# Kernel tuning notes

Measured on AMD Instinct MI355X. Metric: run time of the kernel, lower is better.

Reference implementation:

```python
import jax, jax.numpy as jnp
import numpy as np
import math

B, N, DIM = 8, 8192, 256
DIM_ATTN, HEAD, RANK = 256, 4, 64
HEAD_DIM = DIM_ATTN // HEAD


def setup_inputs() -> dict:
    key = jax.random.key(0)
    ks = jax.random.split(key, 8)
    x = jax.random.normal(ks[0], (B, N, DIM), dtype=jnp.float32)
    z = jax.random.normal(ks[1], (B, N, DIM), dtype=jnp.float32)
    # nn.Linear(dim, dim_attn): weight (out,in) -> use (in,out) for x @ W
    Wq = jax.random.normal(ks[2], (DIM, DIM_ATTN), dtype=jnp.float32) / np.sqrt(DIM)
    bq = jnp.zeros((DIM_ATTN,), dtype=jnp.float32)
    K = jax.random.normal(ks[3], (RANK, HEAD, HEAD_DIM), dtype=jnp.float32)
    Wv = jax.random.normal(ks[4], (DIM, DIM), dtype=jnp.float32) / np.sqrt(DIM)
    bv = jnp.zeros((DIM,), dtype=jnp.float32)
    alpha = jnp.full((HEAD, 1), math.log(9.0), dtype=jnp.float32)
    beta = jnp.full((HEAD, 1), math.log(0.01), dtype=jnp.float32)
    return {"x": x, "z": z, "Wq": Wq, "bq": bq, "K": K, "Wv": Wv, "bv": bv,
            "alpha": alpha, "beta": beta}


def reference(x, z, Wq, bq, K, Wv, bv, alpha, beta):
    b, n, f = x.shape
    # q: (b, n, head, head_dim)
    q = (z @ Wq + bq).reshape(b, n, HEAD, HEAD_DIM)
    # attn scores over latent rank: (b, n, h, r)
    attn = jnp.einsum('bnhd,rhd->bnhr', q, K) / np.sqrt(HEAD_DIM).astype(np.float32)
    # value projection: (b, n, h, d)
    xv = (x @ Wv + bv).reshape(b, n, HEAD, HEAD_DIM)
    # pool over n with softmax over r: (b, r, h, d)
    pooled = jnp.einsum('bnhr,bnhd->brhd', jax.nn.softmax(attn, axis=-1), xv)
    # redistribute with softmax over n: (b, n, h, d)
    v = jnp.einsum('bnhr,brhd->bnhd', jax.nn.softmax(attn, axis=1), pooled)
    # sigmoid-gated combine; alpha/beta are (head, 1) broadcasting over (h, d)
    out = jax.nn.sigmoid(alpha) * xv + jax.nn.sigmoid(beta) * v
    return out.reshape(b, n, f)
```

## Files before the change

### kernel.cpp

```cpp
#include <hip/hip_runtime.h>
#include <hip/hip_bf16.h>

typedef __hip_bfloat16 bf16;
typedef __attribute__((ext_vector_type(8))) __bf16 bf16x8;
typedef __attribute__((ext_vector_type(4))) float f32x4;

#define BB 8
#define NN 8192
#define DIM 256
#define HEAD 4
#define HD 64
#define RANK 64
#define BN (BB*NN)

__device__ __forceinline__ float b2f(bf16 v){ return __bfloat162float(v); }
__device__ __forceinline__ bf16 f2b(float v){ return __float2bfloat16(v); }
__device__ __forceinline__ unsigned short f2bu(float f){
    bf16 h = __float2bfloat16(f);
    return *(unsigned short*)&h;
}
__device__ __forceinline__ float u2f(unsigned short u){
    unsigned int x = ((unsigned int)u) << 16; return __uint_as_float(x);
}
__device__ __forceinline__ __bf16 f2bb(float f){
    bf16 h = __float2bfloat16(f);
    return *reinterpret_cast<__bf16*>(&h);
}
__device__ __forceinline__ int swz(int k, int outer){
    return (((k >> 3) ^ (outer & 7)) << 3) | (k & 7);
}

__global__ void __launch_bounds__(256) kW(
    const float* __restrict__ Wq, const float* __restrict__ bq,
    const float* __restrict__ Km, const float* __restrict__ Wv,
    unsigned short* __restrict__ WattnT, unsigned short* __restrict__ WvT,
    float* __restrict__ battn)
{
    const int c = blockIdx.x;
    const int h = c >> 6, r = c & 63;
    const int t = threadIdx.x;
    __shared__ float Ks[64];
    if(t < 64) Ks[t] = Km[((size_t)r*HEAD + h)*64 + t];
    __syncthreads();

    const float* wqrow = Wq + (size_t)t*DIM + h*64;
    float a = 0.f;
    #pragma unroll
    for(int d = 0; d < 64; d++) a = fmaf(wqrow[d], Ks[d], a);
    WattnT[(size_t)c*DIM + t] = f2bu(0.125f * a);
    WvT[(size_t)c*DIM + t]    = f2bu(Wv[(size_t)t*DIM + c]);
    if(t == 0){
        float bb = 0.f;
        for(int d = 0; d < 64; d++) bb += bq[h*64+d]*Ks[d];
        battn[c] = 0.125f * bb;
    }
}

__global__ void __launch_bounds__(256) kA2(
    const float* __restrict__ A, const unsigned short* __restrict__ WT,
    const float* __restrict__ bias,
    float* __restrict__ outF, unsigned short* __restrict__ outB,
    float* __restrict__ Pm, float* __restrict__ Ps, const int bf16out)
{
    __shared__ __attribute__((aligned(16))) __bf16 As[64][40];
    __shared__ __attribute__((aligned(16))) __bf16 Ws[256][40];

    const int t    = threadIdx.x;
    const int lane = t & 63;
    const int w    = t >> 6;
    const int q    = lane >> 4;
    const int l15  = lane & 15;
    const int brow = blockIdx.x * 64;

    f32x4 acc[4][4];
    #pragma unroll
    for(int tm = 0; tm < 4; tm++)
        #pragma unroll
        for(int tn = 0; tn < 4; tn++) acc[tm][tn] = (f32x4){0.f,0.f,0.f,0.f};

    const int arow = t >> 2, aseg = t & 3;

    for(int k0 = 0; k0 < DIM; k0 += 32){
        {
            const float* ap = A + (size_t)(brow + arow)*DIM + k0 + aseg*8;
            float4 v0 = *(const float4*)(ap + 0);
            float4 v1 = *(const float4*)(ap + 4);
            __attribute__((aligned(16))) __bf16 tmp[8] = {
                f2bb(v0.x), f2bb(v0.y), f2bb(v0.z), f2bb(v0.w),
                f2bb(v1.x), f2bb(v1.y), f2bb(v1.z), f2bb(v1.w)};
            *(bf16x8*)&As[arow][aseg*8] = *(bf16x8*)tmp;
        }
        #pragma unroll
        for(int ii = 0; ii < 4; ii++){
            int c = t + 256*ii;
            int n = c >> 2, seg = c & 3;
            uint4 wv = *(const uint4*)(WT + (size_t)n*DIM + k0 + seg*8);
            *(uint4*)&Ws[n][seg*8] = wv;
        }
        __syncthreads();

        bf16x8 af[4], bf[4];
        #pragma unroll
        for(int tm = 0; tm < 4; tm++) af[tm] = *(const bf16x8*)&As[tm*16 + l15][q*8];
        #pragma unroll
        for(int tn = 0; tn < 4; tn++) bf[tn] = *(const bf16x8*)&Ws[w*64 + tn*16 + l15][q*8];
        #pragma unroll
        for(int tm = 0; tm < 4; tm++)
            #pragma unroll
            for(int tn = 0; tn < 4; tn++)
                acc[tm][tn] = __builtin_amdgcn_mfma_f32_16x16x32_bf16(
                    af[tm], bf[tn], acc[tm][tn], 0, 0, 0);
        __syncthreads();
    }

    if(bf16out){
        const int b  = brow >> 13;
        const int nb = brow & 8191;
        const size_t blk = blockIdx.x;
        #pragma unroll
        for(int tn = 0; tn < 4; tn++){
            int col = w*64 + tn*16 + l15;
            int hh = col >> 6, rr = col & 63;
            float bcol = bias[col];
            float rv[16];
            float m16 = -1e30f;
            #pragma unroll
            for(int tm = 0; tm < 4; tm++){
                #pragma unroll
                for(int reg = 0; reg < 4; reg++){
                    float v = acc[tm][tn][reg] + bcol;
                    unsigned short ub = f2bu(v);
                    int n = nb + tm*16 + q*4 + reg;
                    outB[(((size_t)(b*HEAD + hh))*NN + n)*64 + rr] = ub;
                    float vr = u2f(ub);
                    rv[tm*4+reg] = vr;
                    m16 = fmaxf(m16, vr);
                }
            }
            float s16 = 0.f;
            #pragma unroll
            for(int i = 0; i < 16; i++) s16 += __expf(rv[i] - m16);
            #pragma unroll
            for(int off = 16; off <= 32; off <<= 1){
                float m2 = __shfl_xor(m16, off, 64);
                float s2 = __shfl_xor(s16, off, 64);
                float nm = fmaxf(m16, m2);
                s16 = s16*__expf(m16-nm) + s2*__expf(m2-nm);
                m16 = nm;
            }
            if(q == 0){
                Pm[blk*256 + col] = m16;
                Ps[blk*256 + col] = s16;
            }
        }
    } else {
        #pragma unroll
        for(int tn = 0; tn < 4; tn++){
            int col = w*64 + tn*16 + l15;
            float bcol = bias[col];
            #pragma unroll
            for(int tm = 0; tm < 4; tm++){
                #pragma unroll
                for(int reg = 0; reg < 4; reg++){
                    int grow = brow + tm*16 + q*4 + reg;
                    outF[(size_t)grow*256 + col] = acc[tm][tn][reg] + bcol;
                }
            }
        }
    }
}

__global__ void __launch_bounds__(256) kC(const float* __restrict__ Pm, const float* __restrict__ Ps,
                                          float* __restrict__ M, float* __restrict__ S)
{
    const int b = blockIdx.x, col = threadIdx.x;
    float m = -1e30f;
    for(int c = 0; c < 128; c++)
        m = fmaxf(m, Pm[(size_t)(b*128 + c)*256 + col]);
    float s = 0.f;
    for(int c = 0; c < 128; c++){
        size_t i = (size_t)(b*128 + c)*256 + col;
        s += Ps[i] * __expf(Pm[i] - m);
    }
    M[b*256 + col] = m;
    S[b*256 + col] = s;
}

__global__ void __launch_bounds__(256) kD(const unsigned short* __restrict__ attn,
                                          const float* __restrict__ xv,
                                          float* __restrict__ pooledT)
{
    __shared__ unsigned short s1T[64*256];
    __shared__ unsigned short xvT[64*256];

    const int t = threadIdx.x, lane = t & 63, w = t >> 6;
    const int bh = blockIdx.x, chunk = blockIdx.y;
    const int b = bh >> 2, h = bh & 3;
    const int n0 = chunk * 256;
    const int row = t;

    {
        const uint4* ap = (const uint4*)(attn + ((size_t)bh*NN + n0 + row)*64);
        uint4 ar[8];
        #pragma unroll
        for(int c = 0; c < 8; c++) ar[c] = ap[c];
        float vals[64];
        #pragma unroll
        for(int c = 0; c < 8; c++){
            unsigned int uu[4] = {ar[c].x, ar[c].y, ar[c].z, ar[c].w};
            #pragma unroll
            for(int p = 0; p < 4; p++){
                vals[c*8 + p*2 + 0] = __uint_as_float(uu[p] << 16);
                vals[c*8 + p*2 + 1] = __uint_as_float(uu[p] & 0xffff0000u);
            }
        }
        float mx = -1e30f;
        #pragma unroll
        for(int r = 0; r < 64; r++) mx = fmaxf(mx, vals[r]);
        float s = 0.f;
        #pragma unroll
        for(int r = 0; r < 64; r++){
            float e = __expf(vals[r] - mx);
            s += e;
            s1T[r*256 + swz(row, r)] = f2bu(e);
        }
        float rs = 1.f / s;
        const float4* xp = (const float4*)(xv + ((size_t)(b*NN + n0 + row))*256 + h*64);
        #pragma unroll
        for(int c = 0; c < 16; c++){
            float4 f = xp[c];
            int d0 = c*4;
            xvT[(d0+0)*256 + swz(row, d0+0)] = f2bu(f.x * rs);
            xvT[(d0+1)*256 + swz(row, d0+1)] = f2bu(f.y * rs);
            xvT[(d0+2)*256 + swz(row, d0+2)] = f2bu(f.z * rs);
            xvT[(d0+3)*256 + swz(row, d0+3)] = f2bu(f.w * rs);
        }
    }
    __syncthreads();

    const int q = lane >> 4, l15 = lane & 15;
    const int dm = w*16 + l15;
    f32x4 acc[4];
    #pragma unroll
    for(int tn = 0; tn < 4; tn++) acc[tn] = (f32x4){0.f,0.f,0.f,0.f};

    #pragma unroll
    for(int slab = 0; slab < 8; slab++){
        int c = slab*4 + q;
        bf16x8 a = *(const bf16x8*)&xvT[dm*256 + ((c ^ (dm & 7))<<3)];
        #pragma unroll
        for(int tn = 0; tn < 4; tn++){
            int rn = tn*16 + l15;
            bf16x8 bb = *(const bf16x8*)&s1T[rn*256 + ((c ^ (rn & 7))<<3)];
            acc[tn] = __builtin_amdgcn_mfma_f32_16x16x32_bf16(a, bb, acc[tn], 0, 0, 0);
        }
    }
    #pragma unroll
    for(int tn = 0; tn < 4; tn++){
        #pragma unroll
        for(int reg = 0; reg < 4; reg++){
            int d = w*16 + q*4 + reg;
            int r = tn*16 + l15;
            atomicAdd(&pooledT[((size_t)bh*64 + d)*64 + r], acc[tn][reg]);
        }
    }
}

__global__ void __launch_bounds__(256) kE(const unsigned short* __restrict__ attn,
                                          const float* __restrict__ xvin,
                                          const float* __restrict__ pooledT,
                                          const float* __restrict__ Mst, const float* __restrict__ Sst,
                                          const float* __restrict__ alpha, const float* __restrict__ beta,
                                          float* __restrict__ out)
{
    __shared__ unsigned short s2t[256*64];
    __shared__ unsigned short plT[64*64];
    __shared__ float Ms[64], Sinv[64];

    const int t = threadIdx.x, lane = t & 63, w = t >> 6;
    const int bh = blockIdx.x, chunk = blockIdx.y;
    const int b = bh >> 2, h = bh & 3;
    const int n0 = chunk * 256;
    const int row = t;

    if(t < 64){
        Ms[t]   = Mst[b*256 + h*64 + t];
        Sinv[t] = 1.f / Sst[b*256 + h*64 + t];
    }
    {
        int d = t >> 2, seg = t & 3;
        const float4* pp = (const float4*)(pooledT + ((size_t)bh*64 + d)*64 + seg*16);
        float4 p0 = pp[0], p1 = pp[1], p2 = pp[2], p3 = pp[3];
        __attribute__((aligned(16))) unsigned short tmp[16] = {
            f2bu(p0.x),f2bu(p0.y),f2bu(p0.z),f2bu(p0.w),
            f2bu(p1.x),f2bu(p1.y),f2bu(p1.z),f2bu(p1.w),
            f2bu(p2.x),f2bu(p2.y),f2bu(p2.z),f2bu(p2.w),
            f2bu(p3.x),f2bu(p3.y),f2bu(p3.z),f2bu(p3.w)};
        int c0 = seg*2;
        *(uint4*)&plT[d*64 + (((c0+0) ^ (d&7))<<3)] = *(uint4*)&tmp[0];
        *(uint4*)&plT[d*64 + (((c0+1) ^ (d&7))<<3)] = *(uint4*)&tmp[8];
    }
    __syncthreads();

    {
        const uint4* ap = (const uint4*)(attn + ((size_t)bh*NN + n0 + row)*64);
        #pragma unroll
        for(int c = 0; c < 8; c++){
            uint4 u = ap[c];
            unsigned int uu[4] = {u.x, u.y, u.z, u.w};
            unsigned int ov[4];
            #pragma unroll
            for(int p = 0; p < 4; p++){
                int r = c*8 + p*2;
                float v0 = __uint_as_float(uu[p] << 16);
                float v1 = __uint_as_float(uu[p] & 0xffff0000u);
                float e0 = __expf(v0 - Ms[r])   * Sinv[r];
                float e1 = __expf(v1 - Ms[r+1]) * Sinv[r+1];
                ov[p] = (unsigned int)f2bu(e0) | ((unsigned int)f2bu(e1) << 16);
            }
            uint4 w4; w4.x = ov[0]; w4.y = ov[1]; w4.z = ov[2]; w4.w = ov[3];
            *(uint4*)&s2t[row*64 + ((c ^ (row&7))<<3)] = w4;
        }
    }
    __syncthreads();

    const int q = lane >> 4, l15 = lane & 15;
    f32x4 acc[4][4];
    #pragma unroll
    for(int tm = 0; tm < 4; tm++)
        #pragma unroll
        for(int tn = 0; tn < 4; tn++) acc[tm][tn] = (f32x4){0.f,0.f,0.f,0.f};

    #pragma unroll
    for(int s = 0; s < 2; s++){
        int c = s*4 + q;
        bf16x8 bfr[4], af[4];
        #pragma unroll
        for(int tn = 0; tn < 4; tn++){
            int dn = tn*16 + l15;
            bfr[tn] = *(const bf16x8*)&plT[dn*64 + ((c ^ (dn&7))<<3)];
        }
        #pragma unroll
        for(int tm = 0; tm < 4; tm++){
            int ra = w*64 + tm*16 + l15;
            af[tm] = *(const bf16x8*)&s2t[ra*64 + ((c ^ (ra&7))<<3)];
        }
        #pragma unroll
        for(int tm = 0; tm < 4; tm++)
            #pragma unroll
            for(int tn = 0; tn < 4; tn++)
                acc[tm][tn] = __builtin_amdgcn_mfma_f32_16x16x32_bf16(
                    af[tm], bfr[tn], acc[tm][tn], 0, 0, 0);
    }

    const float sa = 1.f / (1.f + __expf(-alpha[h]));
    const float sb = 1.f / (1.f + __expf(-beta[h]));
    #pragma unroll
    for(int tm = 0; tm < 4; tm++){
        #pragma unroll
        for(int reg = 0; reg < 4; reg++){
            int rowo = w*64 + tm*16 + q*4 + reg;
            size_t gbase = ((size_t)(b*NN + n0 + rowo))*256 + h*64;
            #pragma unroll
            for(int tn = 0; tn < 4; tn++){
                int d = tn*16 + l15;
                out[gbase + d] = sa*xvin[gbase + d] + sb*acc[tm][tn][reg];
            }
        }
    }
}

extern "C" void kernel_launch(void* const* d_in, const int* in_sizes, int n_in,
                              void* d_out, int out_size, void* d_ws, size_t ws_size,
                              hipStream_t stream)
{
    (void)in_sizes; (void)n_in; (void)out_size; (void)ws_size;
    const float* x     = (const float*)d_in[0];
    const float* z     = (const float*)d_in[1];
    const float* Wq    = (const float*)d_in[2];
    const float* bq    = (const float*)d_in[3];
    const float* Km    = (const float*)d_in[4];
    const float* Wv    = (const float*)d_in[5];
    const float* bv    = (const float*)d_in[6];
    const float* alpha = (const float*)d_in[7];
    const float* beta  = (const float*)d_in[8];
    float* out = (float*)d_out;

    float* xv = out;

    char* ws = (char*)d_ws;
    unsigned short* attn  = (unsigned short*)(ws + 0);
    float* pooledT = (float*)(ws + 33554432);
    float* Mst     = (float*)(ws + 34078720);
    float* Sst     = (float*)(ws + 34086912);
    float* Pm      = (float*)(ws + 34095104);
    float* Ps      = (float*)(ws + 35143680);
    unsigned short* WattnT = (unsigned short*)(ws + 36192256);
    unsigned short* WvT    = (unsigned short*)(ws + 36323328);
    float* battn   = (float*)(ws + 36454400);

    (void)hipMemsetAsync(pooledT, 0, 524288, stream);
    kW<<<dim3(256), 256, 0, stream>>>(Wq, bq, Km, Wv, WattnT, WvT, battn);
    kA2<<<dim3(BN/64), 256, 0, stream>>>(x, WvT, bv, xv, nullptr, nullptr, nullptr, 0);
    kA2<<<dim3(BN/64), 256, 0, stream>>>(z, WattnT, battn, nullptr, attn, Pm, Ps, 1);
    kC<<<dim3(8), 256, 0, stream>>>(Pm, Ps, Mst, Sst);
    kD<<<dim3(32, 32), 256, 0, stream>>>(attn, xv, pooledT);
    kE<<<dim3(32, 32), 256, 0, stream>>>(attn, xv, pooledT, Mst, Sst, alpha, beta, out);
}
```

Measured before the change: 295.0 us.

## Load GEMM fragments directly from global memory, removing LDS staging and barriers

The projection GEMM kernel no longer stages A and W tiles through shared memory with two __syncthreads per k-step. Each wave now loads its MFMA fragments straight from global memory (A as fp32, converted to bf16 in registers) and the k-loop is unrolled by two. This removes the LDS traffic and barriers, but each of the four waves redundantly loads the same A rows, which raises global/L2 traffic and lowers load coalescing.

```diff
diff --git a/kernel.cpp b/kernel.cpp
--- a/kernel.cpp
+++ b/kernel.cpp
@@ -62,9 +62,6 @@
     float* __restrict__ outF, unsigned short* __restrict__ outB,
     float* __restrict__ Pm, float* __restrict__ Ps, const int bf16out)
 {
-    __shared__ __attribute__((aligned(16))) __bf16 As[64][40];
-    __shared__ __attribute__((aligned(16))) __bf16 Ws[256][40];
-
     const int t    = threadIdx.x;
     const int lane = t & 63;
     const int w    = t >> 6;
@@ -78,39 +75,35 @@
         #pragma unroll
         for(int tn = 0; tn < 4; tn++) acc[tm][tn] = (f32x4){0.f,0.f,0.f,0.f};
 
-    const int arow = t >> 2, aseg = t & 3;
-
+    const float*          aBase = A  + (size_t)(brow + l15)*DIM + q*8;
+    const unsigned short* bBase = WT + (size_t)(w*64 + l15)*DIM + q*8;
+
+    #pragma unroll 2
     for(int k0 = 0; k0 < DIM; k0 += 32){
-        {
-            const float* ap = A + (size_t)(brow + arow)*DIM + k0 + aseg*8;
-            float4 v0 = *(const float4*)(ap + 0);
-            float4 v1 = *(const float4*)(ap + 4);
+        bf16x8 bfr[4];
+        #pragma unroll
+        for(int tn = 0; tn < 4; tn++)
+            bfr[tn] = *(const bf16x8*)(bBase + (size_t)tn*16*DIM + k0);
+
+        float4 av[4][2];
+        #pragma unroll
+        for(int tm = 0; tm < 4; tm++){
+            const float* ap = aBase + (size_t)tm*16*DIM + k0;
+            av[tm][0] = *(const float4*)(ap + 0);
+            av[tm][1] = *(const float4*)(ap + 4);
+        }
+
+        #pragma unroll
+        for(int tm = 0; tm < 4; tm++){
             __attribute__((aligned(16))) __bf16 tmp[8] = {
-                f2bb(v0.x), f2bb(v0.y), f2bb(v0.z), f2bb(v0.w),
-                f2bb(v1.x), f2bb(v1.y), f2bb(v1.z), f2bb(v1.w)};
-            *(bf16x8*)&As[arow][aseg*8] = *(bf16x8*)tmp;
-        }
-        #pragma unroll
-        for(int ii = 0; ii < 4; ii++){
-            int c = t + 256*ii;
-            int n = c >> 2, seg = c & 3;
-            uint4 wv = *(const uint4*)(WT + (size_t)n*DIM + k0 + seg*8);
-            *(uint4*)&Ws[n][seg*8] = wv;
-        }
-        __syncthreads();
-
-        bf16x8 af[4], bf[4];
-        #pragma unroll
-        for(int tm = 0; tm < 4; tm++) af[tm] = *(const bf16x8*)&As[tm*16 + l15][q*8];
-        #pragma unroll
-        for(int tn = 0; tn < 4; tn++) bf[tn] = *(const bf16x8*)&Ws[w*64 + tn*16 + l15][q*8];
-        #pragma unroll
-        for(int tm = 0; tm < 4; tm++)
+                f2bb(av[tm][0].x), f2bb(av[tm][0].y), f2bb(av[tm][0].z), f2bb(av[tm][0].w),
+                f2bb(av[tm][1].x), f2bb(av[tm][1].y), f2bb(av[tm][1].z), f2bb(av[tm][1].w)};
+            bf16x8 af = *(bf16x8*)tmp;
             #pragma unroll
             for(int tn = 0; tn < 4; tn++)
                 acc[tm][tn] = __builtin_amdgcn_mfma_f32_16x16x32_bf16(
-                    af[tm], bf[tn], acc[tm][tn], 0, 0, 0);
-        __syncthreads();
+                    af, bfr[tn], acc[tm][tn], 0, 0, 0);
+        }
     }
 
     if(bf16out){
```

Result: slower. 336.2 us (+14.0%).

## Double-buffer A tile and load weight fragments directly from global into registers

Applied to the files above, without the earlier changes.

The projection GEMM kernel now double-buffers the A tile in shared memory and prefetches the next slice of A into registers. Weight fragments are read straight from global memory into registers, one step ahead, so the shared-memory weight tile and its staging are gone. This halves the barriers per k-step and overlaps global loads with MFMA work. The cost is extra register pressure and uncoalesced per-lane weight reads that depend on L2/L1 hits.

```diff
diff --git a/kernel.cpp b/kernel.cpp
--- a/kernel.cpp
+++ b/kernel.cpp
@@ -62,8 +62,7 @@
     float* __restrict__ outF, unsigned short* __restrict__ outB,
     float* __restrict__ Pm, float* __restrict__ Ps, const int bf16out)
 {
-    __shared__ __attribute__((aligned(16))) __bf16 As[64][40];
-    __shared__ __attribute__((aligned(16))) __bf16 Ws[256][40];
+    __shared__ __attribute__((aligned(16))) __bf16 As[2][64][40];
 
     const int t    = threadIdx.x;
     const int lane = t & 63;
@@ -79,37 +78,59 @@
         for(int tn = 0; tn < 4; tn++) acc[tm][tn] = (f32x4){0.f,0.f,0.f,0.f};
 
     const int arow = t >> 2, aseg = t & 3;
-
-    for(int k0 = 0; k0 < DIM; k0 += 32){
-        {
-            const float* ap = A + (size_t)(brow + arow)*DIM + k0 + aseg*8;
-            float4 v0 = *(const float4*)(ap + 0);
-            float4 v1 = *(const float4*)(ap + 4);
-            __attribute__((aligned(16))) __bf16 tmp[8] = {
-                f2bb(v0.x), f2bb(v0.y), f2bb(v0.z), f2bb(v0.w),
-                f2bb(v1.x), f2bb(v1.y), f2bb(v1.z), f2bb(v1.w)};
-            *(bf16x8*)&As[arow][aseg*8] = *(bf16x8*)tmp;
-        }
-        #pragma unroll
-        for(int ii = 0; ii < 4; ii++){
-            int c = t + 256*ii;
-            int n = c >> 2, seg = c & 3;
-            uint4 wv = *(const uint4*)(WT + (size_t)n*DIM + k0 + seg*8);
-            *(uint4*)&Ws[n][seg*8] = wv;
-        }
-        __syncthreads();
-
-        bf16x8 af[4], bf[4];
-        #pragma unroll
-        for(int tm = 0; tm < 4; tm++) af[tm] = *(const bf16x8*)&As[tm*16 + l15][q*8];
-        #pragma unroll
-        for(int tn = 0; tn < 4; tn++) bf[tn] = *(const bf16x8*)&Ws[w*64 + tn*16 + l15][q*8];
+    const float* aSrc = A + (size_t)(brow + arow)*DIM + aseg*8;
+    const unsigned short* bBase = WT + (size_t)(w*64 + l15)*DIM + q*8;
+
+    {
+        float4 v0 = *(const float4*)(aSrc + 0);
+        float4 v1 = *(const float4*)(aSrc + 4);
+        __attribute__((aligned(16))) __bf16 tmp[8] = {
+            f2bb(v0.x), f2bb(v0.y), f2bb(v0.z), f2bb(v0.w),
+            f2bb(v1.x), f2bb(v1.y), f2bb(v1.z), f2bb(v1.w)};
+        *(bf16x8*)&As[0][arow][aseg*8] = *(bf16x8*)tmp;
+    }
+    float4 s0 = *(const float4*)(aSrc + 32);
+    float4 s1 = *(const float4*)(aSrc + 36);
+    bf16x8 bcur[4];
+    #pragma unroll
+    for(int tn = 0; tn < 4; tn++)
+        bcur[tn] = *(const bf16x8*)(bBase + (size_t)tn*16*DIM);
+    __syncthreads();
+
+    #pragma unroll
+    for(int step = 0; step < 8; step++){
+        const int cur = step & 1;
+        const int k0  = step * 32;
+
+        bf16x8 bnext[4];
+        if(step < 7){
+            #pragma unroll
+            for(int tn = 0; tn < 4; tn++)
+                bnext[tn] = *(const bf16x8*)(bBase + (size_t)tn*16*DIM + k0 + 32);
+        }
+
+        bf16x8 af[4];
+        #pragma unroll
+        for(int tm = 0; tm < 4; tm++) af[tm] = *(const bf16x8*)&As[cur][tm*16 + l15][q*8];
         #pragma unroll
         for(int tm = 0; tm < 4; tm++)
             #pragma unroll
             for(int tn = 0; tn < 4; tn++)
                 acc[tm][tn] = __builtin_amdgcn_mfma_f32_16x16x32_bf16(
-                    af[tm], bf[tn], acc[tm][tn], 0, 0, 0);
+                    af[tm], bcur[tn], acc[tm][tn], 0, 0, 0);
+
+        if(step < 7){
+            __attribute__((aligned(16))) __bf16 tmp[8] = {
+                f2bb(s0.x), f2bb(s0.y), f2bb(s0.z), f2bb(s0.w),
+                f2bb(s1.x), f2bb(s1.y), f2bb(s1.z), f2bb(s1.w)};
+            *(bf16x8*)&As[cur^1][arow][aseg*8] = *(bf16x8*)tmp;
+        }
+        if(step < 6){
+            s0 = *(const float4*)(aSrc + (step+2)*32 + 0);
+            s1 = *(const float4*)(aSrc + (step+2)*32 + 4);
+        }
+        #pragma unroll
+        for(int tn = 0; tn < 4; tn++) bcur[tn] = bnext[tn];
         __syncthreads();
     }
 
```

Result: no change. 296.6 us (+0.5%).
